# Performance work log

Hardware: AMD Instinct MI355X
Metric: run time of the kernel (lower is better)

Reference implementation:

```python
import jax, jax.numpy as jnp
import numpy as np

H = 12        # num_heads
BLOCK = 128   # sliding-window block_size (include_adjacent=True)
EPS = 1e-5


def layer_norm(x, s, b):
    m = x.mean(-1, keepdims=True)
    v = ((x - m) ** 2).mean(-1, keepdims=True)
    return (x - m) * jax.lax.rsqrt(v + EPS) * s + b


def setup_inputs() -> dict:
    key = jax.random.key(0)
    V, D, F, L, B, S, C = 32000, 768, 3072, 4, 8, 1024, 2
    ks = jax.random.split(key, 10)
    r = lambda k, shp: jax.random.normal(k, shp, dtype=jnp.float32) * 0.02
    return {
        "tokens": jax.random.randint(ks[0], (B, S), 0, V),
        "mask": jnp.ones((B, S), dtype=jnp.int32),
        "emb": r(ks[1], (V, D)),
        "in_w": r(ks[2], (L, 3 * D, D)),
        "in_b": jnp.zeros((L, 3 * D), jnp.float32),
        "out_w": r(ks[3], (L, D, D)),
        "out_b": jnp.zeros((L, D), jnp.float32),
        "ln1_s": jnp.ones((L, D), jnp.float32),
        "ln1_b": jnp.zeros((L, D), jnp.float32),
        "ln2_s": jnp.ones((L, D), jnp.float32),
        "ln2_b": jnp.zeros((L, D), jnp.float32),
        "ff_w1": r(ks[4], (L, F, D)),
        "ff_b1": jnp.zeros((L, F), jnp.float32),
        "ff_w2": r(ks[5], (L, D, F)),
        "ff_b2": jnp.zeros((L, D), jnp.float32),
        "pool_w": r(ks[6], (1, D)),
        "pool_b": jnp.zeros((1,), jnp.float32),
        "cls_ln_s": jnp.ones((D,), jnp.float32),
        "cls_ln_b": jnp.zeros((D,), jnp.float32),
        "cls_w1": r(ks[7], (D, D)),
        "cls_b1": jnp.zeros((D,), jnp.float32),
        "cls_w2": r(ks[8], (C, D)),
        "cls_b2": jnp.zeros((C,), jnp.float32),
    }


def reference(tokens, mask, emb, in_w, in_b, out_w, out_b, ln1_s, ln1_b, ln2_s, ln2_b,
              ff_w1, ff_b1, ff_w2, ff_b2, pool_w, pool_b, cls_ln_s, cls_ln_b,
              cls_w1, cls_b1, cls_w2, cls_b2):
    B, S = tokens.shape
    D = emb.shape[1]
    L = in_w.shape[0]
    hd = D // H
    neg = jnp.finfo(jnp.float32).min

    x = emb[tokens]  # [B,S,D]
    # sinusoidal positional encoding (eval mode: dropout = identity)
    pos = jnp.arange(S, dtype=jnp.float32)[:, None]
    div = jnp.exp(jnp.arange(0, D, 2, dtype=jnp.float32) * (-np.log(10000.0) / D))
    pe = (jnp.zeros((S, D), jnp.float32)
          .at[:, 0::2].set(jnp.sin(pos * div))
          .at[:, 1::2].set(jnp.cos(pos * div)))
    x = x + pe[None]

    idx = jnp.arange(S)
    band = jnp.abs(idx[None, :] - idx[:, None]) <= BLOCK        # [S,S] allowed band
    kpm = (mask != 0)                                            # [B,S] valid keys
    allowed = band[None] & kpm[:, None, :]                       # [B,S,S]

    all_w = []
    for l in range(L):
        h = layer_norm(x, ln1_s[l], ln1_b[l])
        qkv = h @ in_w[l].T + in_b[l]                            # [B,S,3D]
        q, k, v = jnp.split(qkv, 3, axis=-1)
        q = q.reshape(B, S, H, hd).transpose(0, 2, 1, 3) * (1.0 / np.sqrt(hd))
        k = k.reshape(B, S, H, hd).transpose(0, 2, 1, 3)
        v = v.reshape(B, S, H, hd).transpose(0, 2, 1, 3)
        scores = jnp.einsum('bhqd,bhkd->bhqk', q, k)             # [B,H,S,S]
        scores = jnp.where(allowed[:, None], scores, neg)
        w = jax.nn.softmax(scores, axis=-1)
        attn = jnp.einsum('bhqk,bhkd->bhqd', w, v)
        attn = attn.transpose(0, 2, 1, 3).reshape(B, S, D)
        attn = attn @ out_w[l].T + out_b[l]
        x = x + attn
        h2 = layer_norm(x, ln2_s[l], ln2_b[l])
        ff = jax.nn.gelu(h2 @ ff_w1[l].T + ff_b1[l], approximate=False)
        ff = ff @ ff_w2[l].T + ff_b2[l]
        x = x + ff
        all_w.append(w.mean(axis=1))                             # head-averaged [B,S,S]

    # attention pooling
    sc = (x @ pool_w.T + pool_b)[..., 0]                         # [B,S]
    sc = jnp.where(mask == 0, neg, sc)
    pw = jax.nn.softmax(sc, axis=-1)[..., None]
    pooled = jnp.sum(pw * x, axis=1)                             # [B,D]
    pooled = jnp.tanh(pooled)
    c = layer_norm(pooled, cls_ln_s, cls_ln_b)
    c = jnp.tanh(c @ cls_w1.T + cls_b1)
    out = c @ cls_w2.T + cls_b2                                  # [B,2]
    return out, jnp.stack(all_w)
```

## Files before the change

### kernel.cpp

```cpp
#include <hip/hip_runtime.h>
#include <math.h>

#define S_LEN 1024
#define D_MODEL 768
#define NHEAD 12
#define NEG_INF -3.4028234663852886e38f

#define QT 32
#define KB 288

typedef _Float16 f16x8 __attribute__((ext_vector_type(8)));
typedef __attribute__((ext_vector_type(4))) float f32x4;

typedef const __attribute__((address_space(1))) unsigned int ga_u32;
typedef __attribute__((address_space(3))) unsigned int ls_u32;
__device__ __forceinline__ void gload16(const void* g, void* l) {
  __builtin_amdgcn_global_load_lds((ga_u32*)g, (ls_u32*)l, 16, 0, 0);
}

__device__ __forceinline__ float gelu_exact(float v) {
  return 0.5f * v * (1.0f + erff(v * 0.7071067811865475f));
}
__device__ __forceinline__ unsigned short f2h(float f) {
  union { _Float16 h; unsigned short u; } x; x.h = (_Float16)f; return x.u;
}

__global__ __launch_bounds__(256) void embed_kernel(
    const int* __restrict__ tok, const float* __restrict__ emb,
    float* __restrict__ X, int total) {
  int i = blockIdx.x * 256 + threadIdx.x;
  if (i >= total) return;
  int d = i % D_MODEL;
  int bs = i / D_MODEL;
  int s = bs & (S_LEN - 1);
  int t = tok[bs];
  float div = expf((float)(d & ~1) * (-9.210340371976184f / 768.0f));
  float ang = (float)s * div;
  float pe = (d & 1) ? cosf(ang) : sinf(ang);
  X[i] = emb[(size_t)t * D_MODEL + d] + pe;
}

__global__ __launch_bounds__(256) void cvt_w_h(
    const float* __restrict__ W, unsigned short* __restrict__ H, int n4) {
  int i = blockIdx.x * 256 + threadIdx.x;
  if (i >= n4) return;
  float4 w = ((const float4*)W)[i];
  ushort4 h;
  h.x = f2h(w.x); h.y = f2h(w.y); h.z = f2h(w.z); h.w = f2h(w.w);
  ((ushort4*)H)[i] = h;
}

__global__ __launch_bounds__(256) void ln_kernel(
    const float* __restrict__ X, const float* __restrict__ gam,
    const float* __restrict__ bet, unsigned short* __restrict__ Y) {
  __shared__ float scratch[4];
  const int row = blockIdx.x;
  const int tid = threadIdx.x;
  const float* xr = X + (size_t)row * D_MODEL;
  float v0 = xr[tid], v1 = xr[tid + 256], v2 = xr[tid + 512];
  float s = v0 + v1 + v2;
#pragma unroll
  for (int o = 32; o; o >>= 1) s += __shfl_xor(s, o, 64);
  if ((tid & 63) == 0) scratch[tid >> 6] = s;
  __syncthreads();
  float mean = (scratch[0] + scratch[1] + scratch[2] + scratch[3]) * (1.0f / 768.0f);
  __syncthreads();
  float d0 = v0 - mean, d1 = v1 - mean, d2 = v2 - mean;
  float ss = d0 * d0 + d1 * d1 + d2 * d2;
#pragma unroll
  for (int o = 32; o; o >>= 1) ss += __shfl_xor(ss, o, 64);
  if ((tid & 63) == 0) scratch[tid >> 6] = ss;
  __syncthreads();
  float var = (scratch[0] + scratch[1] + scratch[2] + scratch[3]) * (1.0f / 768.0f);
  float rstd = rsqrtf(var + 1e-5f);
  unsigned short* yr = Y + (size_t)row * D_MODEL;
  yr[tid]       = f2h(d0 * rstd * gam[tid]       + bet[tid]);
  yr[tid + 256] = f2h(d1 * rstd * gam[tid + 256] + bet[tid + 256]);
  yr[tid + 512] = f2h(d2 * rstd * gam[tid + 512] + bet[tid + 512]);
}

template <int EPI>
__global__ __launch_bounds__(256) void gemm128(
    const unsigned short* __restrict__ A, const unsigned short* __restrict__ W,
    const float* __restrict__ bias, unsigned short* __restrict__ C,
    int N, int K, int NX) {
  __shared__ __align__(16) unsigned short SH[16384];
  const int tid = threadIdx.x;
  const int nwg = gridDim.x;
  const int wg = ((blockIdx.x & 7) * (nwg >> 3)) + (blockIdx.x >> 3);
  const int ty = wg / NX, tx = wg - ty * NX;
  const int m0 = ty << 7, n0 = tx << 7;
  const int wave = tid >> 6, lane = tid & 63;
  const int wr = (wave >> 1) << 6, wc = (wave & 1) << 6;
  const int lq = lane >> 4, lr = lane & 15;
  const int rA0 = (wave << 5) + (lane >> 2);
  const int rA1 = rA0 + 16;
  const int sl = lane & 3;
  const size_t gA0 = (size_t)(m0 + rA0) * K + ((sl ^ ((rA0 >> 1) & 3)) << 3);
  const size_t gA1 = (size_t)(m0 + rA1) * K + ((sl ^ ((rA1 >> 1) & 3)) << 3);
  const size_t gB0 = (size_t)(n0 + rA0) * K + ((sl ^ ((rA0 >> 1) & 3)) << 3);
  const size_t gB1 = (size_t)(n0 + rA1) * K + ((sl ^ ((rA1 >> 1) & 3)) << 3);
  const int lws = wave << 10;

  const int nt = K >> 5;
  {
    unsigned short* base = SH;
    gload16(A + gA0, base + lws);
    gload16(A + gA1, base + lws + 512);
    gload16(W + gB0, base + 4096 + lws);
    gload16(W + gB1, base + 4096 + lws + 512);
  }
  __syncthreads();

  f32x4 acc[4][4] = {};
  int cur = 0;
  for (int t = 0; t < nt; ++t) {
    if (t + 1 < nt) {
      const int kk = (t + 1) << 5;
      unsigned short* base = SH + ((cur ^ 1) << 13);
      gload16(A + gA0 + kk, base + lws);
      gload16(A + gA1 + kk, base + lws + 512);
      gload16(W + gB0 + kk, base + 4096 + lws);
      gload16(W + gB1 + kk, base + 4096 + lws + 512);
    }
    const unsigned short* As = SH + (cur << 13);
    const unsigned short* Bs = As + 4096;
    f16x8 af[4], bq[4];
#pragma unroll
    for (int i = 0; i < 4; ++i) {
      int r = wr + (i << 4) + lr;
      af[i] = *(const f16x8*)&As[r * 32 + ((lq ^ ((r >> 1) & 3)) << 3)];
    }
#pragma unroll
    for (int j = 0; j < 4; ++j) {
      int r = wc + (j << 4) + lr;
      bq[j] = *(const f16x8*)&Bs[r * 32 + ((lq ^ ((r >> 1) & 3)) << 3)];
    }
#pragma unroll
    for (int i = 0; i < 4; ++i)
#pragma unroll
      for (int j = 0; j < 4; ++j)
        acc[i][j] = __builtin_amdgcn_mfma_f32_16x16x32_f16(af[i], bq[j], acc[i][j], 0, 0, 0);
    if (t + 1 < nt) { __syncthreads(); cur ^= 1; }
  }
  float bval[4];
#pragma unroll
  for (int j = 0; j < 4; ++j) bval[j] = bias[n0 + wc + (j << 4) + lr];
  __syncthreads();
#pragma unroll
  for (int hh = 0; hh < 2; ++hh) {
    if ((wave >> 1) == hh) {
#pragma unroll
      for (int i = 0; i < 4; ++i)
#pragma unroll
        for (int j = 0; j < 4; ++j) {
          const int colb = wc + (j << 4) + lr;
#pragma unroll
          for (int r = 0; r < 4; ++r) {
            const int rowl = (i << 4) + (lq << 2) + r;
            float v = acc[i][j][r] + bval[j];
            if (EPI == 1) v = gelu_exact(v);
            const int ch = (colb >> 3) ^ (rowl & 7);
            SH[rowl * 128 + (ch << 3) + (colb & 7)] = f2h(v);
          }
        }
    }
    __syncthreads();
#pragma unroll
    for (int it = 0; it < 4; ++it) {
      const int cid = tid + (it << 8);
      const int row = cid >> 4, ch = cid & 15;
      uint4 v8 = *(uint4*)&SH[row * 128 + ((ch ^ (row & 7)) << 3)];
      *(uint4*)&C[(size_t)(m0 + (hh << 6) + row) * N + n0 + (ch << 3)] = v8;
    }
    __syncthreads();
  }
}

__global__ __launch_bounds__(256) void gemm64r(
    const unsigned short* __restrict__ A, const unsigned short* __restrict__ W,
    const float* __restrict__ bias, float* __restrict__ C, int N, int K, int NX) {
  __shared__ __align__(16) unsigned short SH[12288];
  const int tid = threadIdx.x;
  const int nwg = gridDim.x;
  const int wg = ((blockIdx.x & 7) * (nwg >> 3)) + (blockIdx.x >> 3);
  const int ty = wg / NX, tx = wg - ty * NX;
  const int m0 = ty << 6, n0 = tx << 7;
  const int wave = tid >> 6, lane = tid & 63;
  const int wr = (wave >> 1) << 5, wc = (wave & 1) << 6;
  const int lq = lane >> 4, lr = lane & 15;
  const int rA = (wave << 4) + (lane >> 2);
  const int rB0 = (wave << 5) + (lane >> 2);
  const int rB1 = rB0 + 16;
  const int sl = lane & 3;
  const size_t gA  = (size_t)(m0 + rA) * K + ((sl ^ ((rA >> 1) & 3)) << 3);
  const size_t gB0 = (size_t)(n0 + rB0) * K + ((sl ^ ((rB0 >> 1) & 3)) << 3);
  const size_t gB1 = (size_t)(n0 + rB1) * K + ((sl ^ ((rB1 >> 1) & 3)) << 3);
  const int lwA = wave << 9;
  const int lwB = wave << 10;

  const int nt = K >> 5;
  {
    unsigned short* base = SH;
    gload16(A + gA, base + lwA);
    gload16(W + gB0, base + 2048 + lwB);
    gload16(W + gB1, base + 2048 + lwB + 512);
  }
  __syncthreads();

  f32x4 acc[2][4] = {};
  int cur = 0;
  for (int t = 0; t < nt; ++t) {
    if (t + 1 < nt) {
      const int kk = (t + 1) << 5;
      unsigned short* base = SH + (cur ^ 1) * 6144;
      gload16(A + gA + kk, base + lwA);
      gload16(W + gB0 + kk, base + 2048 + lwB);
      gload16(W + gB1 + kk, base + 2048 + lwB + 512);
    }
    const unsigned short* As = SH + cur * 6144;
    const unsigned short* Bs = As + 2048;
    f16x8 af[2], bq[4];
#pragma unroll
    for (int i = 0; i < 2; ++i) {
      int r = wr + (i << 4) + lr;
      af[i] = *(const f16x8*)&As[r * 32 + ((lq ^ ((r >> 1) & 3)) << 3)];
    }
#pragma unroll
    for (int j = 0; j < 4; ++j) {
      int r = wc + (j << 4) + lr;
      bq[j] = *(const f16x8*)&Bs[r * 32 + ((lq ^ ((r >> 1) & 3)) << 3)];
    }
#pragma unroll
    for (int i = 0; i < 2; ++i)
#pragma unroll
      for (int j = 0; j < 4; ++j)
        acc[i][j] = __builtin_amdgcn_mfma_f32_16x16x32_f16(af[i], bq[j], acc[i][j], 0, 0, 0);
    if (t + 1 < nt) { __syncthreads(); cur ^= 1; }
  }
#pragma unroll
  for (int j = 0; j < 4; ++j) {
    const int gcol = n0 + wc + (j << 4) + lr;
    const float bv = bias[gcol];
#pragma unroll
    for (int i = 0; i < 2; ++i) {
      const int grow0 = m0 + wr + (i << 4) + (lq << 2);
#pragma unroll
      for (int r = 0; r < 4; ++r) {
        size_t off = (size_t)(grow0 + r) * N + gcol;
        C[off] += acc[i][j][r] + bv;
      }
    }
  }
}

__global__ __launch_bounds__(512) void attn_kernel(
    const unsigned short* __restrict__ qkv, const int* __restrict__ mask,
    unsigned short* __restrict__ attn_out, float* __restrict__ allw) {
  __shared__ __align__(16) unsigned short Ks[KB * 72];
  __shared__ __align__(16) unsigned short Vt[64 * 328];
  __shared__ __align__(16) unsigned short Qs[32 * 72];
  __shared__ __align__(16) unsigned short Ps[32 * 328];
  __shared__ __align__(16) float redmax[2][16][4];
  __shared__ __align__(16) float redsum[2][16][4];
  __shared__ int kvalid[KB];

  const int qt0 = blockIdx.x * QT;
  const int b = blockIdx.y;
  const int tid = threadIdx.x;
  const int w = tid >> 6, lane = tid & 63;
  const int lr = lane & 15, lg = lane >> 4;
  const int k0 = qt0 - 128;
  const int qh = w & 1, wq = w >> 1;
  const int nkt = (wq < 2) ? 5 : 4;

  for (int j = tid; j < KB; j += 512) {
    int key = k0 + j;
    kvalid[j] = (key >= 0 && key < S_LEN && mask[b * S_LEN + key] != 0) ? 1 : 0;
  }

  f32x4 pm[5] = {};
  const size_t rowbase = (size_t)(b * S_LEN) * 2304;
  const int qloc = lg << 2;
  const int qbase = (qh << 4) + qloc;

  for (int h = 0; h < NHEAD; ++h) {
    const int hoff = h << 6;
    if (tid < 256) {
      int r = tid >> 3, c = tid & 7;
      uint4 v = *(const uint4*)(qkv + rowbase + (size_t)(qt0 + r) * 2304 + hoff + (c << 3));
      *(uint4*)&Qs[r * 72 + ((c ^ (r & 7)) << 3)] = v;
    }
    for (int idx = tid; idx < 2304; idx += 512) {
      int r = idx >> 3, c = idx & 7;
      int key = k0 + r;
      uint4 kv = {0, 0, 0, 0}, vv = {0, 0, 0, 0};
      if ((unsigned)key < (unsigned)S_LEN) {
        const unsigned short* base = qkv + rowbase + (size_t)key * 2304 + hoff + (c << 3);
        kv = *(const uint4*)(base + 768);
        vv = *(const uint4*)(base + 1536);
      }
      *(uint4*)&Ks[r * 72 + ((c ^ (r & 7)) << 3)] = kv;
      const unsigned short* ve = (const unsigned short*)&vv;
      int jc = r >> 3, jw = r & 7;
#pragma unroll
      for (int e = 0; e < 8; ++e) {
        int d = (c << 3) + e;
        Vt[d * 328 + ((jc ^ ((d >> 2) & 7)) << 3) + jw] = ve[e];
      }
    }
    __syncthreads();

    f16x8 aq[2];
#pragma unroll
    for (int kc = 0; kc < 2; ++kc) {
      int r = (qh << 4) + lr;
      aq[kc] = *(f16x8*)&Qs[r * 72 + ((((kc << 2) + lg) ^ (r & 7)) << 3)];
    }
    f32x4 sc[5];
#pragma unroll
    for (int t = 0; t < 5; ++t) {
      sc[t] = (f32x4){0.0f, 0.0f, 0.0f, 0.0f};
      if (t < nkt) {
        int r = ((wq + (t << 2)) << 4) + lr;
#pragma unroll
        for (int kc = 0; kc < 2; ++kc) {
          f16x8 bk = *(f16x8*)&Ks[r * 72 + ((((kc << 2) + lg) ^ (r & 7)) << 3)];
          sc[t] = __builtin_amdgcn_mfma_f32_16x16x32_f16(aq[kc], bk, sc[t], 0, 0, 0);
        }
      }
    }
#pragma unroll
    for (int t = 0; t < 5; ++t) if (t < nkt) {
      int j = ((wq + (t << 2)) << 4) + lr;
      int okk = kvalid[j];
#pragma unroll
      for (int rg = 0; rg < 4; ++rg) {
        int q = qbase + rg;
        float s = sc[t][rg] * 0.125f;
        sc[t][rg] = (okk && j >= q && j <= q + 256) ? s : NEG_INF;
      }
    }
    float mx[4], zs[4];
#pragma unroll
    for (int rg = 0; rg < 4; ++rg) {
      float m = NEG_INF;
#pragma unroll
      for (int t = 0; t < 5; ++t) if (t < nkt) m = fmaxf(m, sc[t][rg]);
      mx[rg] = m;
    }
#pragma unroll
    for (int o = 1; o < 16; o <<= 1)
#pragma unroll
      for (int rg = 0; rg < 4; ++rg) mx[rg] = fmaxf(mx[rg], __shfl_xor(mx[rg], o, 64));
    if (lr == 0)
#pragma unroll
      for (int rg = 0; rg < 4; ++rg) redmax[qh][qloc + rg][wq] = mx[rg];
    __syncthreads();
#pragma unroll
    for (int rg = 0; rg < 4; ++rg) {
      f32x4 v = *(f32x4*)&redmax[qh][qloc + rg][0];
      mx[rg] = fmaxf(fmaxf(v[0], v[1]), fmaxf(v[2], v[3]));
      zs[rg] = 0.0f;
    }
#pragma unroll
    for (int t = 0; t < 5; ++t) if (t < nkt)
#pragma unroll
      for (int rg = 0; rg < 4; ++rg) {
        float e = expf(sc[t][rg] - mx[rg]);
        sc[t][rg] = e;
        zs[rg] += e;
      }
#pragma unroll
    for (int o = 1; o < 16; o <<= 1)
#pragma unroll
      for (int rg = 0; rg < 4; ++rg) zs[rg] += __shfl_xor(zs[rg], o, 64);
    if (lr == 0)
#pragma unroll
      for (int rg = 0; rg < 4; ++rg) redsum[qh][qloc + rg][wq] = zs[rg];
    __syncthreads();
#pragma unroll
    for (int rg = 0; rg < 4; ++rg) {
      f32x4 v = *(f32x4*)&redsum[qh][qloc + rg][0];
      zs[rg] = 1.0f / (v[0] + v[1] + v[2] + v[3]);
    }
#pragma unroll
    for (int t = 0; t < 5; ++t) if (t < nkt) {
      int j = ((wq + (t << 2)) << 4) + lr;
      int pc = j >> 3, pw = j & 7;
#pragma unroll
      for (int rg = 0; rg < 4; ++rg) {
        float p = sc[t][rg] * zs[rg];
        pm[t][rg] += p;
        int row = qbase + rg;
        Ps[row * 328 + ((pc ^ (row & 7)) << 3) + pw] = f2h(p);
      }
    }
    __syncthreads();
    {
      const int qt = w >> 2, dt = w & 3;
      const int ra = (qt << 4) + lr;
      const int rd = (dt << 4) + lr;
      f32x4 o4 = {0.0f, 0.0f, 0.0f, 0.0f};
#pragma unroll
      for (int ks = 0; ks < 9; ++ks) {
        f16x8 pa = *(f16x8*)&Ps[ra * 328 + ((((ks << 2) + lg) ^ (ra & 7)) << 3)];
        f16x8 vb = *(f16x8*)&Vt[rd * 328 + ((((ks << 2) + lg) ^ ((rd >> 2) & 7)) << 3)];
        o4 = __builtin_amdgcn_mfma_f32_16x16x32_f16(pa, vb, o4, 0, 0, 0);
      }
      unsigned short* op = attn_out +
          ((size_t)(b * S_LEN + qt0 + (qt << 4) + (lg << 2))) * D_MODEL + hoff + (dt << 4) + lr;
#pragma unroll
      for (int rg = 0; rg < 4; ++rg) op[(size_t)rg * D_MODEL] = f2h(o4[rg]);
    }
    __syncthreads();
  }

#pragma unroll
  for (int t = 0; t < 5; ++t) if (t < nkt) {
    int j = ((wq + (t << 2)) << 4) + lr;
    int key = k0 + j;
    if ((unsigned)key < (unsigned)S_LEN) {
      float* ap = allw + ((size_t)(b * S_LEN) + qt0 + qbase) * S_LEN + key;
#pragma unroll
      for (int rg = 0; rg < 4; ++rg) ap[(size_t)rg * S_LEN] = pm[t][rg] * (1.0f / 12.0f);
    }
  }
}

__global__ __launch_bounds__(256) void pool_score(
    const float* __restrict__ X, const int* __restrict__ mask,
    const float* __restrict__ pool_w, const float* __restrict__ pool_b,
    float* __restrict__ sc) {
  const int tid = threadIdx.x;
  const int wave = tid >> 6, lane = tid & 63;
  const int row = blockIdx.x * 4 + wave;
  const float* xr = X + (size_t)row * D_MODEL;
  float acc = 0.0f;
#pragma unroll
  for (int c = 0; c < 3; ++c) {
    int d = (lane << 2) + (c << 8);
    float4 xv = *(const float4*)(xr + d);
    float4 wv = *(const float4*)(pool_w + d);
    acc += xv.x * wv.x + xv.y * wv.y + xv.z * wv.z + xv.w * wv.w;
  }
#pragma unroll
  for (int o = 32; o; o >>= 1) acc += __shfl_xor(acc, o, 64);
  if (lane == 0)
    sc[row] = (mask[row] == 0) ? NEG_INF : (acc + pool_b[0]);
}

__global__ __launch_bounds__(256) void pool_softmax(float* __restrict__ sc) {
  __shared__ float scratch[4];
  __shared__ float buf[S_LEN];
  const int b = blockIdx.x;
  const int tid = threadIdx.x;
  float* sb = sc + b * S_LEN;
  float m = NEG_INF;
  for (int s = tid; s < S_LEN; s += 256) { buf[s] = sb[s]; m = fmaxf(m, buf[s]); }
#pragma unroll
  for (int o = 32; o; o >>= 1) m = fmaxf(m, __shfl_xor(m, o, 64));
  if ((tid & 63) == 0) scratch[tid >> 6] = m;
  __syncthreads();
  m = fmaxf(fmaxf(scratch[0], scratch[1]), fmaxf(scratch[2], scratch[3]));
  __syncthreads();
  float z = 0.0f;
  for (int s = tid; s < S_LEN; s += 256) { float e = expf(buf[s] - m); buf[s] = e; z += e; }
#pragma unroll
  for (int o = 32; o; o >>= 1) z += __shfl_xor(z, o, 64);
  if ((tid & 63) == 0) scratch[tid >> 6] = z;
  __syncthreads();
  float Z = scratch[0] + scratch[1] + scratch[2] + scratch[3];
  const float inv = 1.0f / Z;
  for (int s = tid; s < S_LEN; s += 256) sb[s] = buf[s] * inv;
}

__global__ __launch_bounds__(256) void pool_sum(
    const float* __restrict__ X, const float* __restrict__ wgt,
    float* __restrict__ partial) {
  const int bx = blockIdx.x;
  const int b = blockIdx.y;
  const int dchunk = bx >> 3, schunk = bx & 7;
  const int d = (dchunk << 8) + threadIdx.x;
  const int s0 = schunk << 7;
  const float* xb = X + ((size_t)(b << 10) + s0) * D_MODEL + d;
  const float* wb = wgt + (b << 10) + s0;
  float acc = 0.0f;
  for (int s = 0; s < 128; ++s) acc += wb[s] * xb[(size_t)s * D_MODEL];
  partial[((size_t)((b << 3) + schunk)) * D_MODEL + d] = acc;
}

__global__ __launch_bounds__(256) void cls_finish(
    const float* __restrict__ partial,
    const float* __restrict__ ln_s, const float* __restrict__ ln_b,
    const float* __restrict__ w1, const float* __restrict__ b1,
    const float* __restrict__ w2, const float* __restrict__ b2,
    float* __restrict__ out) {
  const int b = blockIdx.x;
  const int tid = threadIdx.x;
  __shared__ float scratch[4];
  __shared__ __align__(16) float pbuf[D_MODEL];
  __shared__ __align__(16) float cbuf[D_MODEL];
  __shared__ __align__(16) float c1[D_MODEL];
  for (int d = tid; d < D_MODEL; d += 256) {
    float acc = 0.0f;
#pragma unroll
    for (int p = 0; p < 8; ++p) acc += partial[((size_t)((b << 3) + p)) * D_MODEL + d];
    pbuf[d] = tanhf(acc);
  }
  __syncthreads();
  float ls = 0.0f;
  for (int d = tid; d < D_MODEL; d += 256) ls += pbuf[d];
#pragma unroll
  for (int o = 32; o; o >>= 1) ls += __shfl_xor(ls, o, 64);
  if ((tid & 63) == 0) scratch[tid >> 6] = ls;
  __syncthreads();
  float mean = (scratch[0] + scratch[1] + scratch[2] + scratch[3]) * (1.0f / 768.0f);
  __syncthreads();
  float vs = 0.0f;
  for (int d = tid; d < D_MODEL; d += 256) { float dd = pbuf[d] - mean; vs += dd * dd; }
#pragma unroll
  for (int o = 32; o; o >>= 1) vs += __shfl_xor(vs, o, 64);
  if ((tid & 63) == 0) scratch[tid >> 6] = vs;
  __syncthreads();
  float var = (scratch[0] + scratch[1] + scratch[2] + scratch[3]) * (1.0f / 768.0f);
  float rstd = rsqrtf(var + 1e-5f);
  __syncthreads();
  for (int d = tid; d < D_MODEL; d += 256)
    cbuf[d] = (pbuf[d] - mean) * rstd * ln_s[d] + ln_b[d];
  __syncthreads();
  for (int i = tid; i < D_MODEL; i += 256) {
    const float* wr = w1 + (size_t)i * D_MODEL;
    float acc = 0.0f;
    for (int d = 0; d < D_MODEL; d += 4) {
      float4 wv = *(const float4*)(wr + d);
      float4 cv = *(const float4*)(&cbuf[d]);
      acc += wv.x * cv.x + wv.y * cv.y + wv.z * cv.z + wv.w * cv.w;
    }
    c1[i] = tanhf(acc + b1[i]);
  }
  __syncthreads();
#pragma unroll
  for (int jc = 0; jc < 2; ++jc) {
    float acc = 0.0f;
    for (int i = tid; i < D_MODEL; i += 256) acc += c1[i] * w2[jc * D_MODEL + i];
#pragma unroll
    for (int o = 32; o; o >>= 1) acc += __shfl_xor(acc, o, 64);
    if ((tid & 63) == 0) scratch[tid >> 6] = acc;
    __syncthreads();
    if (tid == 0) out[b * 2 + jc] = scratch[0] + scratch[1] + scratch[2] + scratch[3] + b2[jc];
    __syncthreads();
  }
}

extern "C" void kernel_launch(void* const* d_in, const int* in_sizes, int n_in,
                              void* d_out, int out_size, void* d_ws, size_t ws_size,
                              hipStream_t stream) {
  const int*   tokens  = (const int*)d_in[0];
  const int*   mask    = (const int*)d_in[1];
  const float* emb     = (const float*)d_in[2];
  const float* in_w    = (const float*)d_in[3];
  const float* in_b    = (const float*)d_in[4];
  const float* out_w   = (const float*)d_in[5];
  const float* out_b   = (const float*)d_in[6];
  const float* ln1_s   = (const float*)d_in[7];
  const float* ln1_b   = (const float*)d_in[8];
  const float* ln2_s   = (const float*)d_in[9];
  const float* ln2_b   = (const float*)d_in[10];
  const float* ff_w1   = (const float*)d_in[11];
  const float* ff_b1   = (const float*)d_in[12];
  const float* ff_w2   = (const float*)d_in[13];
  const float* ff_b2   = (const float*)d_in[14];
  const float* pool_w  = (const float*)d_in[15];
  const float* pool_b  = (const float*)d_in[16];
  const float* cls_ln_s = (const float*)d_in[17];
  const float* cls_ln_b = (const float*)d_in[18];
  const float* cls_w1  = (const float*)d_in[19];
  const float* cls_b1  = (const float*)d_in[20];
  const float* cls_w2  = (const float*)d_in[21];
  const float* cls_b2  = (const float*)d_in[22];

  float* outp = (float*)d_out;
  float* ws = (float*)d_ws;
  const size_t XN = (size_t)8 * 1024 * 768;
  const size_t BIGU = (size_t)8192 * 3072;
  float* x = ws;
  unsigned short* bigu = (unsigned short*)(ws + XN);
  unsigned short* h_f16 = (unsigned short*)(ws + XN + BIGU / 2);
  unsigned short* wall = h_f16 + XN;
  unsigned short* wall_in  = wall;
  unsigned short* wall_out = wall + (size_t)7077888;
  unsigned short* wall_ff1 = wall + (size_t)9437184;
  unsigned short* wall_ff2 = wall + (size_t)18874368;
  float* clsbuf = (float*)(wall + (size_t)28311552);
  float* sc_ws = clsbuf;
  float* partial = clsbuf + 8192;
  float* allw = outp + 16;

  hipMemsetAsync(d_out, 0, (size_t)out_size * sizeof(float), stream);

  cvt_w_h<<<6912, 256, 0, stream>>>(in_w,  wall_in,  1769472);
  cvt_w_h<<<2304, 256, 0, stream>>>(out_w, wall_out,  589824);
  cvt_w_h<<<9216, 256, 0, stream>>>(ff_w1, wall_ff1, 2359296);
  cvt_w_h<<<9216, 256, 0, stream>>>(ff_w2, wall_ff2, 2359296);

  const int total = (int)XN;
  embed_kernel<<<(total + 255) / 256, 256, 0, stream>>>(tokens, emb, x, total);

  for (int l = 0; l < 4; ++l) {
    ln_kernel<<<8192, 256, 0, stream>>>(x, ln1_s + l * 768, ln1_b + l * 768, h_f16);
    gemm128<0><<<1152, 256, 0, stream>>>(h_f16, wall_in + (size_t)l * 1769472,
                                         in_b + l * 2304, bigu, 2304, 768, 18);
    attn_kernel<<<dim3(S_LEN / QT, 8), 512, 0, stream>>>(bigu, mask, h_f16,
                                                         allw + (size_t)l * 8 * 1024 * 1024);
    gemm64r<<<768, 256, 0, stream>>>(h_f16, wall_out + (size_t)l * 589824,
                                     out_b + l * 768, x, 768, 768, 6);
    ln_kernel<<<8192, 256, 0, stream>>>(x, ln2_s + l * 768, ln2_b + l * 768, h_f16);
    gemm128<1><<<1536, 256, 0, stream>>>(h_f16, wall_ff1 + (size_t)l * 2359296,
                                         ff_b1 + l * 3072, bigu, 3072, 768, 24);
    gemm64r<<<768, 256, 0, stream>>>(bigu, wall_ff2 + (size_t)l * 2359296,
                                     ff_b2 + l * 768, x, 768, 3072, 6);
  }

  pool_score<<<2048, 256, 0, stream>>>(x, mask, pool_w, pool_b, sc_ws);
  pool_softmax<<<8, 256, 0, stream>>>(sc_ws);
  pool_sum<<<dim3(24, 8), 256, 0, stream>>>(x, sc_ws, partial);
  cls_finish<<<8, 256, 0, stream>>>(partial, cls_ln_s, cls_ln_b,
                                    cls_w1, cls_b1, cls_w2, cls_b2, outp);
}
```

Before: 1.503 ms.

## Triple-buffer GEMM LDS staging with two-tile-deep prefetch and explicit vmcnt waits

Switches both GEMM kernels from double-buffered to triple-buffered shared-memory staging, so global loads run two K-tiles ahead. Fine-grained s_waitcnt vmcnt counts plus raw barriers replace the full __syncthreads after each tile, which should hide more global-load latency behind MFMA work. The cost is 50% more LDS per block, which may reduce occupancy. The hand-set wait counts also depend on the exact number of loads issued per stage.

```diff
diff --git a/kernel.cpp b/kernel.cpp
--- a/kernel.cpp
+++ b/kernel.cpp
@@ -84,7 +84,7 @@
     const unsigned short* __restrict__ A, const unsigned short* __restrict__ W,
     const float* __restrict__ bias, unsigned short* __restrict__ C,
     int N, int K, int NX) {
-  __shared__ __align__(16) unsigned short SH[16384];
+  __shared__ __align__(16) unsigned short SH[24576];
   const int tid = threadIdx.x;
   const int nwg = gridDim.x;
   const int wg = ((blockIdx.x & 7) * (nwg >> 3)) + (blockIdx.x >> 3);
@@ -103,27 +103,32 @@
   const int lws = wave << 10;
 
   const int nt = K >> 5;
-  {
-    unsigned short* base = SH;
-    gload16(A + gA0, base + lws);
-    gload16(A + gA1, base + lws + 512);
-    gload16(W + gB0, base + 4096 + lws);
-    gload16(W + gB1, base + 4096 + lws + 512);
-  }
-  __syncthreads();
+  auto stage = [&](int buf, int t) {
+    unsigned short* base = SH + (buf << 13);
+    const int kk = t << 5;
+    gload16(A + gA0 + kk, base + lws);
+    gload16(A + gA1 + kk, base + lws + 512);
+    gload16(W + gB0 + kk, base + 4096 + lws);
+    gload16(W + gB1 + kk, base + 4096 + lws + 512);
+  };
+  stage(0, 0);
+  stage(1, 1);
 
   f32x4 acc[4][4] = {};
-  int cur = 0;
+  int cb = 0;
   for (int t = 0; t < nt; ++t) {
-    if (t + 1 < nt) {
-      const int kk = (t + 1) << 5;
-      unsigned short* base = SH + ((cur ^ 1) << 13);
-      gload16(A + gA0 + kk, base + lws);
-      gload16(A + gA1 + kk, base + lws + 512);
-      gload16(W + gB0 + kk, base + 4096 + lws);
-      gload16(W + gB1 + kk, base + 4096 + lws + 512);
-    }
-    const unsigned short* As = SH + (cur << 13);
+    if (t + 2 < nt) {
+      int sb = cb + 2; if (sb >= 3) sb -= 3;
+      stage(sb, t + 2);
+      asm volatile("s_waitcnt vmcnt(8)" ::: "memory");
+    } else if (t + 2 == nt) {
+      asm volatile("s_waitcnt vmcnt(4)" ::: "memory");
+    } else {
+      asm volatile("s_waitcnt vmcnt(0)" ::: "memory");
+    }
+    __builtin_amdgcn_s_barrier();
+    __builtin_amdgcn_sched_barrier(0);
+    const unsigned short* As = SH + (cb << 13);
     const unsigned short* Bs = As + 4096;
     f16x8 af[4], bq[4];
 #pragma unroll
@@ -141,7 +146,9 @@
 #pragma unroll
       for (int j = 0; j < 4; ++j)
         acc[i][j] = __builtin_amdgcn_mfma_f32_16x16x32_f16(af[i], bq[j], acc[i][j], 0, 0, 0);
-    if (t + 1 < nt) { __syncthreads(); cur ^= 1; }
+    __builtin_amdgcn_sched_barrier(0);
+    __builtin_amdgcn_s_barrier();
+    cb = (cb == 2) ? 0 : cb + 1;
   }
   float bval[4];
 #pragma unroll
@@ -180,7 +187,7 @@
 __global__ __launch_bounds__(256) void gemm64r(
     const unsigned short* __restrict__ A, const unsigned short* __restrict__ W,
     const float* __restrict__ bias, float* __restrict__ C, int N, int K, int NX) {
-  __shared__ __align__(16) unsigned short SH[12288];
+  __shared__ __align__(16) unsigned short SH[18432];
   const int tid = threadIdx.x;
   const int nwg = gridDim.x;
   const int wg = ((blockIdx.x & 7) * (nwg >> 3)) + (blockIdx.x >> 3);
@@ -200,25 +207,31 @@
   const int lwB = wave << 10;
 
   const int nt = K >> 5;
-  {
-    unsigned short* base = SH;
-    gload16(A + gA, base + lwA);
-    gload16(W + gB0, base + 2048 + lwB);
-    gload16(W + gB1, base + 2048 + lwB + 512);
-  }
-  __syncthreads();
+  auto stage = [&](int buf, int t) {
+    unsigned short* base = SH + buf * 6144;
+    const int kk = t << 5;
+    gload16(A + gA + kk, base + lwA);
+    gload16(W + gB0 + kk, base + 2048 + lwB);
+    gload16(W + gB1 + kk, base + 2048 + lwB + 512);
+  };
+  stage(0, 0);
+  stage(1, 1);
 
   f32x4 acc[2][4] = {};
-  int cur = 0;
+  int cb = 0;
   for (int t = 0; t < nt; ++t) {
-    if (t + 1 < nt) {
-      const int kk = (t + 1) << 5;
-      unsigned short* base = SH + (cur ^ 1) * 6144;
-      gload16(A + gA + kk, base + lwA);
-      gload16(W + gB0 + kk, base + 2048 + lwB);
-      gload16(W + gB1 + kk, base + 2048 + lwB + 512);
-    }
-    const unsigned short* As = SH + cur * 6144;
+    if (t + 2 < nt) {
+      int sb = cb + 2; if (sb >= 3) sb -= 3;
+      stage(sb, t + 2);
+      asm volatile("s_waitcnt vmcnt(6)" ::: "memory");
+    } else if (t + 2 == nt) {
+      asm volatile("s_waitcnt vmcnt(3)" ::: "memory");
+    } else {
+      asm volatile("s_waitcnt vmcnt(0)" ::: "memory");
+    }
+    __builtin_amdgcn_s_barrier();
+    __builtin_amdgcn_sched_barrier(0);
+    const unsigned short* As = SH + cb * 6144;
     const unsigned short* Bs = As + 2048;
     f16x8 af[2], bq[4];
 #pragma unroll
@@ -236,7 +249,9 @@
 #pragma unroll
       for (int j = 0; j < 4; ++j)
         acc[i][j] = __builtin_amdgcn_mfma_f32_16x16x32_f16(af[i], bq[j], acc[i][j], 0, 0, 0);
-    if (t + 1 < nt) { __syncthreads(); cur ^= 1; }
+    __builtin_amdgcn_sched_barrier(0);
+    __builtin_amdgcn_s_barrier();
+    cb = (cb == 2) ? 0 : cb + 1;
   }
 #pragma unroll
   for (int j = 0; j < 4; ++j) {
```

After: 1.479 ms. About the same (-1.6%).
